# Optimization experiments

Hardware: AMD Instinct MI355X
Metric: run time of the kernel (lower is better)

## Reference

```python
import jax, jax.numpy as jnp
import numpy as np

B = 2048          # batch of latent vectors
NW = 32           # n_windows = floor(4096 / 128)
D = 128           # split_size == window_size == codebook dim
K = 2048          # codebook entries


def setup_inputs() -> dict:
    key = jax.random.key(0)
    k1, k2 = jax.random.split(key)
    ze = jax.random.normal(k1, (B, NW * D), dtype=jnp.float32)
    codebook = jax.random.normal(k2, (K, D), dtype=jnp.float32)
    return {"ze": ze, "codebook": codebook}


def reference(ze, codebook):
    # Window-based VQ: original loops over NW windows of width D along the
    # last axis; contiguous equal-width slices == reshape, so vectorize.
    Kc, Dc = codebook.shape
    zw = ze.reshape(ze.shape[0], -1, Dc)                      # [B, NW, D]
    # squared distances: ||z||^2 + ||c||^2 - 2 z.c  -> [B, NW, K]
    sq = (jnp.sum(zw * zw, axis=-1, keepdims=True)
          + jnp.sum(codebook * codebook, axis=1)
          - 2.0 * jnp.einsum('bwd,kd->bwk', zw, codebook))
    idx = jnp.argmin(sq, axis=-1)                             # [B, NW]
    zq = jnp.take(codebook, idx, axis=0)                      # [B, NW, D]
    return zq.reshape(ze.shape)
```

## Files before the change

kernel.cpp:

```cpp
#include <hip/hip_runtime.h>
#include <hip/hip_bf16.h>


#define VQ_D 128
#define VQ_K 2048
#define VQ_M 65536
#define VQ_THR 0.04f

typedef short short8 __attribute__((ext_vector_type(8)));
typedef int  int4v  __attribute__((ext_vector_type(4)));
typedef int  i32x16 __attribute__((ext_vector_type(16)));
typedef unsigned long long u64;

__device__ uint4 g_cbi[VQ_K * 16];
__device__ int   g_list[VQ_M];
__device__ u64   g_res[VQ_M];
__device__ int   g_count;

__global__ void vq_prepn(const float* __restrict__ cb, float2* __restrict__ cs2) {
    int g = blockIdx.x * 256 + threadIdx.x;
    int r = g >> 4, t = g & 15;
    const float4* s = reinterpret_cast<const float4*>(cb) + (size_t)g * 2;
    float4 f0 = s[0], f1 = s[1];
    float z[8] = {f0.x, f0.y, f0.z, f0.w, f1.x, f1.y, f1.z, f1.w};
    float ss = ((z[0]*z[0] + z[1]*z[1]) + (z[2]*z[2] + z[3]*z[3]))
             + ((z[4]*z[4] + z[5]*z[5]) + (z[6]*z[6] + z[7]*z[7]));
    float ax = fmaxf(fmaxf(fmaxf(fabsf(z[0]), fabsf(z[1])), fmaxf(fabsf(z[2]), fabsf(z[3]))),
                     fmaxf(fmaxf(fabsf(z[4]), fabsf(z[5])), fmaxf(fabsf(z[6]), fabsf(z[7]))));
    ss += __shfl_xor(ss, 1); ax = fmaxf(ax, __shfl_xor(ax, 1));
    ss += __shfl_xor(ss, 2); ax = fmaxf(ax, __shfl_xor(ax, 2));
    ss += __shfl_xor(ss, 4); ax = fmaxf(ax, __shfl_xor(ax, 4));
    ss += __shfl_xor(ss, 8); ax = fmaxf(ax, __shfl_xor(ax, 8));
    float mx  = fmaxf(ax, 1e-20f);
    float s1  = mx * (1.0f / 127.0f);
    float inv = 127.0f / mx;
    float inv2 = inv * 256.0f;
    int qa[8], qr[8];
    #pragma unroll
    for (int i = 0; i < 8; ++i) {
        float qf = rintf(z[i] * inv);
        float r1 = fmaf(-qf, s1, z[i]);
        float q2f = fminf(127.f, fmaxf(-127.f, rintf(r1 * inv2)));
        qa[i] = (int)qf; qr[i] = (int)q2f;
    }
    uint2 w1, w2;
    w1.x = (qa[0]&255) | ((qa[1]&255)<<8) | ((qa[2]&255)<<16) | ((unsigned)(qa[3]&255)<<24);
    w1.y = (qa[4]&255) | ((qa[5]&255)<<8) | ((qa[6]&255)<<16) | ((unsigned)(qa[7]&255)<<24);
    w2.x = (qr[0]&255) | ((qr[1]&255)<<8) | ((qr[2]&255)<<16) | ((unsigned)(qr[3]&255)<<24);
    w2.y = (qr[4]&255) | ((qr[5]&255)<<8) | ((qr[6]&255)<<16) | ((unsigned)(qr[7]&255)<<24);
    uint2* cw = reinterpret_cast<uint2*>(g_cbi);
    int c1 = (t >> 1) ^ (r & 15);
    int c2 = (8 + (t >> 1)) ^ (r & 15);
    cw[(r * 16 + c1) * 2 + (t & 1)] = w1;
    cw[(r * 16 + c2) * 2 + (t & 1)] = w2;
    if (t == 0) cs2[r] = make_float2(ss, s1);
    if (g == 0) g_count = 0;
}

__global__ __launch_bounds__(256, 2)
void vq_score(const float* __restrict__ ze,
              const float2* __restrict__ cs2,
              int* __restrict__ outIdx) {
    __shared__ uint4 sB[4096];
    const int tid  = threadIdx.x;
    const int lane = tid & 63;
    const int wv   = tid >> 6;
    const int ln31 = lane & 31;
    const int g2   = lane >> 5;
    const int qb   = blockIdx.x * 128;

    uint2 q1w[8], q2w[8];
    float s1r[8];
    #pragma unroll
    for (int jj = 0; jj < 8; ++jj) {
        int id = wv * 512 + jj * 64 + lane, r = id >> 4, t = id & 15;
        const float4* src =
            reinterpret_cast<const float4*>(ze + (size_t)(qb + r) * VQ_D + t * 8);
        float4 f0 = src[0], f1 = src[1];
        float z[8] = {f0.x, f0.y, f0.z, f0.w, f1.x, f1.y, f1.z, f1.w};
        float ax = fmaxf(fmaxf(fmaxf(fabsf(z[0]), fabsf(z[1])), fmaxf(fabsf(z[2]), fabsf(z[3]))),
                         fmaxf(fmaxf(fabsf(z[4]), fabsf(z[5])), fmaxf(fabsf(z[6]), fabsf(z[7]))));
        ax = fmaxf(ax, __shfl_xor(ax, 1));
        ax = fmaxf(ax, __shfl_xor(ax, 2));
        ax = fmaxf(ax, __shfl_xor(ax, 4));
        ax = fmaxf(ax, __shfl_xor(ax, 8));
        float mx  = fmaxf(ax, 1e-20f);
        float s1  = mx * (1.0f / 127.0f);
        float inv = 127.0f / mx;
        float inv2 = inv * 256.0f;
        s1r[jj] = s1;
        int qa[8], qr[8];
        #pragma unroll
        for (int i = 0; i < 8; ++i) {
            float qf = rintf(z[i] * inv);
            float r1 = fmaf(-qf, s1, z[i]);
            float q2f = fminf(127.f, fmaxf(-127.f, rintf(r1 * inv2)));
            qa[i] = (int)qf; qr[i] = (int)q2f;
        }
        q1w[jj].x = (qa[0]&255) | ((qa[1]&255)<<8) | ((qa[2]&255)<<16) | ((unsigned)(qa[3]&255)<<24);
        q1w[jj].y = (qa[4]&255) | ((qa[5]&255)<<8) | ((qa[6]&255)<<16) | ((unsigned)(qa[7]&255)<<24);
        q2w[jj].x = (qr[0]&255) | ((qr[1]&255)<<8) | ((qr[2]&255)<<16) | ((unsigned)(qr[3]&255)<<24);
        q2w[jj].y = (qr[4]&255) | ((qr[5]&255)<<8) | ((qr[6]&255)<<16) | ((unsigned)(qr[7]&255)<<24);
    }
    {
        uint2* sw = reinterpret_cast<uint2*>(sB);
        #pragma unroll
        for (int jj = 0; jj < 8; ++jj) {
            int id = wv * 512 + jj * 64 + lane, r = id >> 4, t = id & 15;
            int c1 = (t >> 1) ^ (r & 15);
            int c2 = (8 + (t >> 1)) ^ (r & 15);
            sw[(r * 16 + c1) * 2 + (t & 1)] = q1w[jj];
            sw[(r * 16 + c2) * 2 + (t & 1)] = q2w[jj];
        }
    }
    float mj[16];
    #pragma unroll
    for (int j = 0; j < 16; ++j) {
        float va = __shfl(s1r[2 * (j >> 2)],     (j & 3) << 4);
        float vb = __shfl(s1r[2 * (j >> 2) + 1], (j & 3) << 4);
        mj[j] = (g2 ? vb : va) * (-1.0f / 128.0f);
    }
    __syncthreads();
    int4v aq1[4], aq2[4];
    {
        int r = wv * 32 + ln31;
        #pragma unroll
        for (int kc = 0; kc < 4; ++kc) {
            int c = kc * 2 + g2;
            aq1[kc] = *(const int4v*)&sB[r * 16 + (c ^ (r & 15))];
            aq2[kc] = *(const int4v*)&sB[r * 16 + ((8 + c) ^ (r & 15))];
        }
    }
    __syncthreads();

    #define STAGE_B(T, BUF)                                                     \
        _Pragma("unroll")                                                       \
        for (int jj = 0; jj < 8; ++jj) {                                        \
            int base = wv * 512 + jj * 64;                                      \
            __builtin_amdgcn_global_load_lds(                                   \
                (const void*)(g_cbi + (size_t)(T) * 2048 + base + lane),        \
                (void*)(sB + (BUF) * 2048 + base), 16, 0, 0);                   \
        }
    STAGE_B(0, 0)

    float m1[16], m2[16];
    int   i1[16];
    #pragma unroll
    for (int j = 0; j < 16; ++j) { m1[j] = 3.0e38f; m2[j] = 3.0e38f; i1[j] = 0; }

    const int x15 = ln31 & 15;

    for (int tile = 0; tile < VQ_K / 128; ++tile) {
        asm volatile("s_waitcnt vmcnt(0)" ::: "memory");
        __builtin_amdgcn_s_barrier();
        __builtin_amdgcn_sched_barrier(0);

        const int bb = (tile & 1) << 11;

        if (tile < VQ_K / 128 - 1) { STAGE_B(tile + 1, (tile + 1) & 1) }

        #pragma unroll
        for (int col = 0; col < 4; ++col) {
            const int cr = col * 32 + ln31;
            const int kb = tile * 128 + cr;
            float2 cf = cs2[kb];

            i32x16 HH, XX;
            #pragma unroll
            for (int j = 0; j < 16; ++j) { HH[j] = 0; XX[j] = 0; }

            __builtin_amdgcn_s_setprio(1);
            #pragma unroll
            for (int kc = 0; kc < 4; ++kc) {
                int c  = kc * 2 + g2;
                int p1 = c ^ x15, p2 = (8 + c) ^ x15;
                int4v bh = *(const int4v*)&sB[bb + cr * 16 + p1];
                int4v bl = *(const int4v*)&sB[bb + cr * 16 + p2];
                XX = __builtin_amdgcn_mfma_i32_32x32x32_i8(aq2[kc], bh, XX, 0, 0, 0);
                HH = __builtin_amdgcn_mfma_i32_32x32x32_i8(aq1[kc], bh, HH, 0, 0, 0);
                XX = __builtin_amdgcn_mfma_i32_32x32x32_i8(aq1[kc], bl, XX, 0, 0, 0);
            }
            __builtin_amdgcn_s_setprio(0);

            #pragma unroll
            for (int j = 0; j < 16; ++j) {
                float s0 = fmaf((float)((HH[j] << 8) + XX[j]) * cf.y, mj[j], cf.x);
                bool lt0 = s0 < m1[j];
                m2[j] = lt0 ? m1[j] : fminf(m2[j], s0);
                i1[j] = lt0 ? kb : i1[j];
                m1[j] = lt0 ? s0 : m1[j];
            }
        }
    }

    #pragma unroll
    for (int j = 0; j < 16; ++j) {
        float a1v = m1[j], a2v = m2[j];
        int   ai  = i1[j];
        #pragma unroll
        for (int off = 1; off < 32; off <<= 1) {
            float o1 = __shfl_xor(a1v, off);
            float o2 = __shfl_xor(a2v, off);
            int   oi = __shfl_xor(ai, off);
            bool lt = o1 < a1v;
            float hi = lt ? a1v : o1;
            a1v = lt ? o1 : a1v;
            ai  = lt ? oi : ai;
            a2v = fminf(fminf(a2v, o2), hi);
        }
        if (ln31 == 0) {
            int row = qb + wv * 32 + (j & 3) + 8 * (j >> 2) + 4 * g2;
            if (a2v - a1v < VQ_THR) {
                outIdx[row] = (int)((unsigned)ai | 0x80000000u);
                g_res[row] = ~0ull;
                int pos = atomicAdd(&g_count, 1);
                g_list[pos] = row;
            } else {
                outIdx[row] = ai;
            }
        }
    }
    #undef STAGE_B
}

__global__ __launch_bounds__(256)
void vq_rescue(const float* __restrict__ ze,
               const float* __restrict__ cb,
               const float2* __restrict__ cs2) {
    __shared__ float cs[64 * 132];
    __shared__ float zs[4][128];

    const int tid  = threadIdx.x;
    const int lane = tid & 63;
    const int wv   = tid >> 6;
    const int count = g_count;
    const long nitems = (long)((count + 3) >> 2) * 32;

    for (long it = blockIdx.x; it < nitems; it += gridDim.x) {
        const int grp   = (int)(it >> 5);
        const int chunk = (int)(it & 31);
        const int slot  = grp * 4 + wv;
        const bool valid = slot < count;
        const int row = g_list[valid ? slot : (count - 1)];

        #pragma unroll
        for (int j = 0; j < 8; ++j) {
            int id = j * 256 + tid;
            int r = id >> 5, col = id & 31;
            float4 v = reinterpret_cast<const float4*>(cb)[(size_t)(chunk * 64 + r) * 32 + col];
            *reinterpret_cast<float4*>(&cs[r * 132 + col * 4]) = v;
        }
        if (tid < 128) {
            int w = tid >> 5, i = tid & 31;
            int s2 = grp * 4 + w; if (s2 >= count) s2 = count - 1;
            int rw = g_list[s2];
            float4 v = reinterpret_cast<const float4*>(ze)[(size_t)rw * 32 + i];
            *reinterpret_cast<float4*>(&zs[w][i * 4]) = v;
        }
        __syncthreads();

        if (valid) {
            float4 zn = {0.f, 0.f, 0.f, 0.f};
            #pragma unroll
            for (int i = 0; i < 32; ++i) {
                float4 z = *reinterpret_cast<const float4*>(&zs[wv][i * 4]);
                zn.x += z.x * z.x; zn.y += z.y * z.y;
                zn.z += z.z * z.z; zn.w += z.w * z.w;
            }
            float znorm = (zn.x + zn.y) + (zn.z + zn.w);

            int k = chunk * 64 + lane;
            float4 a = {0.f, 0.f, 0.f, 0.f};
            #pragma unroll
            for (int i = 0; i < 32; ++i) {
                float4 c = *reinterpret_cast<const float4*>(&cs[lane * 132 + i * 4]);
                float4 z = *reinterpret_cast<const float4*>(&zs[wv][i * 4]);
                a.x += z.x * c.x; a.y += z.y * c.y;
                a.z += z.z * c.z; a.w += z.w * c.w;
            }
            float dot = (a.x + a.y) + (a.z + a.w);
            float s = fmaf(-2.f, dot, znorm + cs2[k].x);

            u64 p = ((u64)__float_as_uint(s) << 32) | (unsigned)k;
            #pragma unroll
            for (int o = 1; o < 64; o <<= 1) {
                u64 q = __shfl_xor(p, o);
                p = q < p ? q : p;
            }
            if (lane == 0) atomicMin(&g_res[row], p);
        }
        __syncthreads();
    }
}

__global__ void vq_gather(const float* __restrict__ cb,
                          const int* __restrict__ idx,
                          float* __restrict__ out) {
    size_t u = (size_t)blockIdx.x * blockDim.x + threadIdx.x;
    int r = (int)(u >> 5);
    int j = (int)(u & 31);
    int v = idx[r];
    if (v < 0) v = (int)(g_res[r] & 0xFFFFFFFFull);
    reinterpret_cast<float4*>(out)[u] =
        reinterpret_cast<const float4*>(cb)[((size_t)v << 5) + j];
}

extern "C" void kernel_launch(void* const* d_in, const int* in_sizes, int n_in,
                              void* d_out, int out_size, void* d_ws, size_t ws_size,
                              hipStream_t stream) {
    const float* ze = (const float*)d_in[0];
    const float* cb = (const float*)d_in[1];
    float* out = (float*)d_out;

    float2* cs2  = (float2*)d_ws;
    int*    bidx = (int*)((char*)d_ws + 16384);

    vq_prepn<<<VQ_K * VQ_D / 8 / 256, 256, 0, stream>>>(cb, cs2);
    vq_score<<<VQ_M / 128, 256, 0, stream>>>(ze, cs2, bidx);
    vq_rescue<<<1024, 256, 0, stream>>>(ze, cb, cs2);
    vq_gather<<<(VQ_M * (VQ_D / 4)) / 256, 256, 0, stream>>>(cb, bidx, out);
}
```

Baseline: 115.7 us.

## Halve LDS codebook tile to 64 rows, prefetch norms, use med3 top-2 update

Shrinks the double-buffered codebook tile from 128 to 64 rows, which halves LDS use to 32KB and doubles the number of barrier iterations. Each tile is processed as two explicit 32-column halves. The codebook norm/scale pairs for the next tile are prefetched into registers, and the first MFMA starts from a zero accumulator instead of zeroing registers. The second-best update uses fmed3 and the best value uses fminf. The aim is lower LDS pressure for higher occupancy and shorter per-iteration latency, at the cost of more barriers and waits.

```diff
diff --git a/kernel.cpp b/kernel.cpp
--- a/kernel.cpp
+++ b/kernel.cpp
@@ -61,7 +61,7 @@
 void vq_score(const float* __restrict__ ze,
               const float2* __restrict__ cs2,
               int* __restrict__ outIdx) {
-    __shared__ uint4 sB[4096];
+    __shared__ uint4 sB[2048];
     const int tid  = threadIdx.x;
     const int lane = tid & 63;
     const int wv   = tid >> 6;
@@ -135,11 +135,11 @@
 
     #define STAGE_B(T, BUF)                                                     \
         _Pragma("unroll")                                                       \
-        for (int jj = 0; jj < 8; ++jj) {                                        \
-            int base = wv * 512 + jj * 64;                                      \
+        for (int jj = 0; jj < 4; ++jj) {                                        \
+            int base = wv * 256 + jj * 64;                                      \
             __builtin_amdgcn_global_load_lds(                                   \
-                (const void*)(g_cbi + (size_t)(T) * 2048 + base + lane),        \
-                (void*)(sB + (BUF) * 2048 + base), 16, 0, 0);                   \
+                (const void*)(g_cbi + (size_t)(T) * 1024 + base + lane),        \
+                (void*)(sB + (BUF) * 1024 + base), 16, 0, 0);                   \
         }
     STAGE_B(0, 0)
 
@@ -148,34 +148,46 @@
     #pragma unroll
     for (int j = 0; j < 16; ++j) { m1[j] = 3.0e38f; m2[j] = 3.0e38f; i1[j] = 0; }
 
+    i32x16 Z;
+    #pragma unroll
+    for (int j = 0; j < 16; ++j) Z[j] = 0;
+
+    float2 cf0 = cs2[ln31];
+    float2 cf1 = cs2[32 + ln31];
     const int x15 = ln31 & 15;
 
-    for (int tile = 0; tile < VQ_K / 128; ++tile) {
+    for (int tile = 0; tile < VQ_K / 64; ++tile) {
         asm volatile("s_waitcnt vmcnt(0)" ::: "memory");
         __builtin_amdgcn_s_barrier();
         __builtin_amdgcn_sched_barrier(0);
 
-        const int bb = (tile & 1) << 11;
-
-        if (tile < VQ_K / 128 - 1) { STAGE_B(tile + 1, (tile + 1) & 1) }
-
-        #pragma unroll
-        for (int col = 0; col < 4; ++col) {
-            const int cr = col * 32 + ln31;
-            const int kb = tile * 128 + cr;
-            float2 cf = cs2[kb];
-
+        const int bb = (tile & 1) << 10;
+
+        if (tile < VQ_K / 64 - 1) { STAGE_B(tile + 1, (tile + 1) & 1) }
+        int nt = (tile + 1) & (VQ_K / 64 - 1);
+        float2 nf0 = cs2[nt * 64 + ln31];
+        float2 nf1 = cs2[nt * 64 + 32 + ln31];
+
+        int kb = tile * 64 + ln31;
+
+        {
             i32x16 HH, XX;
-            #pragma unroll
-            for (int j = 0; j < 16; ++j) { HH[j] = 0; XX[j] = 0; }
-
             __builtin_amdgcn_s_setprio(1);
-            #pragma unroll
-            for (int kc = 0; kc < 4; ++kc) {
+            {
+                int c  = g2;
+                int p1 = c ^ x15, p2 = (8 + c) ^ x15;
+                int4v bh = *(const int4v*)&sB[bb + ln31 * 16 + p1];
+                int4v bl = *(const int4v*)&sB[bb + ln31 * 16 + p2];
+                XX = __builtin_amdgcn_mfma_i32_32x32x32_i8(aq2[0], bh, Z, 0, 0, 0);
+                HH = __builtin_amdgcn_mfma_i32_32x32x32_i8(aq1[0], bh, Z, 0, 0, 0);
+                XX = __builtin_amdgcn_mfma_i32_32x32x32_i8(aq1[0], bl, XX, 0, 0, 0);
+            }
+            #pragma unroll
+            for (int kc = 1; kc < 4; ++kc) {
                 int c  = kc * 2 + g2;
                 int p1 = c ^ x15, p2 = (8 + c) ^ x15;
-                int4v bh = *(const int4v*)&sB[bb + cr * 16 + p1];
-                int4v bl = *(const int4v*)&sB[bb + cr * 16 + p2];
+                int4v bh = *(const int4v*)&sB[bb + ln31 * 16 + p1];
+                int4v bl = *(const int4v*)&sB[bb + ln31 * 16 + p2];
                 XX = __builtin_amdgcn_mfma_i32_32x32x32_i8(aq2[kc], bh, XX, 0, 0, 0);
                 HH = __builtin_amdgcn_mfma_i32_32x32x32_i8(aq1[kc], bh, HH, 0, 0, 0);
                 XX = __builtin_amdgcn_mfma_i32_32x32x32_i8(aq1[kc], bl, XX, 0, 0, 0);
@@ -184,13 +196,49 @@
 
             #pragma unroll
             for (int j = 0; j < 16; ++j) {
-                float s0 = fmaf((float)((HH[j] << 8) + XX[j]) * cf.y, mj[j], cf.x);
+                float s0 = fmaf((float)((HH[j] << 8) + XX[j]) * cf0.y, mj[j], cf0.x);
                 bool lt0 = s0 < m1[j];
-                m2[j] = lt0 ? m1[j] : fminf(m2[j], s0);
+                m2[j] = __builtin_amdgcn_fmed3f(s0, m1[j], m2[j]);
                 i1[j] = lt0 ? kb : i1[j];
-                m1[j] = lt0 ? s0 : m1[j];
-            }
-        }
+                m1[j] = fminf(m1[j], s0);
+            }
+        }
+
+        {
+            i32x16 HH, XX;
+            __builtin_amdgcn_s_setprio(1);
+            {
+                int c  = g2;
+                int p1 = c ^ x15, p2 = (8 + c) ^ x15;
+                int4v bh = *(const int4v*)&sB[bb + (32 + ln31) * 16 + p1];
+                int4v bl = *(const int4v*)&sB[bb + (32 + ln31) * 16 + p2];
+                XX = __builtin_amdgcn_mfma_i32_32x32x32_i8(aq2[0], bh, Z, 0, 0, 0);
+                HH = __builtin_amdgcn_mfma_i32_32x32x32_i8(aq1[0], bh, Z, 0, 0, 0);
+                XX = __builtin_amdgcn_mfma_i32_32x32x32_i8(aq1[0], bl, XX, 0, 0, 0);
+            }
+            #pragma unroll
+            for (int kc = 1; kc < 4; ++kc) {
+                int c  = kc * 2 + g2;
+                int p1 = c ^ x15, p2 = (8 + c) ^ x15;
+                int4v bh = *(const int4v*)&sB[bb + (32 + ln31) * 16 + p1];
+                int4v bl = *(const int4v*)&sB[bb + (32 + ln31) * 16 + p2];
+                XX = __builtin_amdgcn_mfma_i32_32x32x32_i8(aq2[kc], bh, XX, 0, 0, 0);
+                HH = __builtin_amdgcn_mfma_i32_32x32x32_i8(aq1[kc], bh, HH, 0, 0, 0);
+                XX = __builtin_amdgcn_mfma_i32_32x32x32_i8(aq1[kc], bl, XX, 0, 0, 0);
+            }
+            __builtin_amdgcn_s_setprio(0);
+
+            #pragma unroll
+            for (int j = 0; j < 16; ++j) {
+                float s1v = fmaf((float)((HH[j] << 8) + XX[j]) * cf1.y, mj[j], cf1.x);
+                bool lt1 = s1v < m1[j];
+                m2[j] = __builtin_amdgcn_fmed3f(s1v, m1[j], m2[j]);
+                i1[j] = lt1 ? kb + 32 : i1[j];
+                m1[j] = fminf(m1[j], s1v);
+            }
+        }
+
+        cf0 = nf0; cf1 = nf1;
     }
 
     #pragma unroll
```

Result: faster. 112.6 us (-2.7%).
